# Optimization experiments

Hardware: AMD Instinct MI355X
Metric: run time of the kernel (lower is better)

## Reference

```python
import jax, jax.numpy as jnp
import numpy as np


def setup_inputs() -> dict:
    key = jax.random.key(0)
    D, H, T, B = 512, 512, 500, 128
    ks = jax.random.split(key, 12)
    tn = lambda k, shape: 0.01 * jax.random.truncated_normal(k, -2.0, 2.0, shape, dtype=jnp.float32)
    return {
        "inputs": jax.random.normal(ks[0], (B, D), dtype=jnp.float32),
        "Wz": tn(ks[1], (D, H)),
        "Wr": tn(ks[2], (D, H)),
        "Wh": tn(ks[3], (D, H)),
        "Uz": tn(ks[4], (H, H)),
        "Ur": tn(ks[5], (H, H)),
        "Uh": tn(ks[6], (H, H)),
        "bz": tn(ks[7], (H,)),
        "br": tn(ks[8], (H,)),
        "bh": tn(ks[9], (H,)),
        "Wo": tn(ks[10], (H, D)),
        "bo": tn(ks[11], (D,)),
        "T": T,
    }


def reference(inputs, Wz, Wr, Wh, Uz, Ur, Uh, bz, br, bh, Wo, bo, T):
    B, D = inputs.shape
    H = Wz.shape[1]

    def step(carry, _):
        h, x = carry  # h: [B,H], x: [B,D]
        r = jax.nn.sigmoid(x @ Wr + h @ Ur + br)
        h_prop = jnp.tanh(x @ Wh + (r * h) @ Uh + bh)
        z = jax.nn.sigmoid(x @ Wz + h @ Uz + bz)
        h_new = jnp.clip((1.0 - z) * h + z * h_prop, -5.0, 5.0)
        out = h_new @ Wo + bo
        return (h_new, out), out

    h0 = jnp.zeros((B, H), dtype=inputs.dtype)
    _, outs = jax.lax.scan(step, (h0, inputs), None, length=T - 1)  # [T-1,B,D]
    full = jnp.concatenate([inputs[None], outs], axis=0)  # [T,B,D]
    return jnp.transpose(full, (1, 0, 2))  # [B,T,D]
```

## Files before the change

### kernel.cpp

```cpp
#include <hip/hip_runtime.h>
#include <cstdint>

#define NB 128
#define DH 512
#define ROWS 528

#define OFF_M   0u
#define OFF_M1  1048576u
#define OFF_UH  2097152u
#define OFF_H   2359296u
#define OFF_RH  2426880u
#define OFF_XT  2494464u
#define OFF_GZ  2562048u
#define OFF_GH  2627584u
#define OFF_CV  2693120u
#define OFF_C1  2695168u
#define OFF_BAR 2697216u
#define OFF_H2  2701312u

__device__ __forceinline__ float sigm(float x) { return 1.f / (1.f + __expf(-x)); }
__device__ __forceinline__ float tanh_fast(float x) {
  float e = __expf(2.f * fminf(x, 40.f));
  return (e - 1.f) / (e + 1.f);
}

__device__ __forceinline__ float cload(const float* p) {
  return __hip_atomic_load(p, __ATOMIC_RELAXED, __HIP_MEMORY_SCOPE_AGENT);
}
__device__ __forceinline__ void cstore(float* p, float v) {
  __hip_atomic_store(p, v, __ATOMIC_RELAXED, __HIP_MEMORY_SCOPE_AGENT);
}

__global__ __launch_bounds__(256) void gru_pre(
    const float* __restrict__ inputs,
    const float* __restrict__ Wz, const float* __restrict__ Wr, const float* __restrict__ Wh,
    const float* __restrict__ Uz, const float* __restrict__ Ur, const float* __restrict__ Uh,
    const float* __restrict__ bz, const float* __restrict__ br, const float* __restrict__ bh,
    const float* __restrict__ Wo, const float* __restrict__ bo,
    float* __restrict__ ws)
{
  __shared__ float sh[8960];
  const int bid = blockIdx.x, t = threadIdx.x;
  float* Mw  = ws + OFF_M;
  float* M1w = ws + OFF_M1;
  float* Uhw = ws + OFF_UH;
  float* hw0 = ws + OFF_H;
  float* hw1 = ws + OFF_H2;
  float* rhw = ws + OFF_RH;
  float* xT  = ws + OFF_XT;
  float* cv  = ws + OFF_CV;
  float* c1  = ws + OFF_C1;
  uint32_t* bar = (uint32_t*)(ws + OFF_BAR);

  if (bid < 256) {
    const int kh = bid >> 7, cch = bid & 127;
    const int reg = cch >> 5;
    const int k0 = kh * 256, c0 = cch * 16;
    if (reg == 3) {
      const int cc0 = c0 - 1536;
      for (int i = 0; i < 16; ++i) {
        int idx = t + i * 256;
        int kk = k0 + (idx >> 4), ci = idx & 15;
        Mw[(cch * 512 + kk) * 16 + ci] = Wo[kk * 512 + cc0 + ci];
      }
    } else {
      const float* Ws = (reg == 0) ? Wr : (reg == 1) ? Wz : Wh;
      const float* Us = (reg == 0) ? Ur : (reg == 1) ? Uz : nullptr;
      const int cc0 = c0 - reg * 512;
      const int kl = t;
      const int k = k0 + kl;
      float acc[16];
      #pragma unroll
      for (int c = 0; c < 16; ++c) acc[c] = 0.f;
      for (int jt = 0; jt < 16; ++jt) {
        __syncthreads();
        for (int i = 0; i < 32; ++i) {
          int idx = t + i * 256;
          int kk = idx >> 5, jj = idx & 31;
          sh[kk * 35 + jj] = Wo[(k0 + kk) * 512 + jt * 32 + jj];
        }
        __syncthreads();
        for (int j = 0; j < 32; ++j) {
          float wv = sh[kl * 35 + j];
          const float* wrow = Ws + (jt * 32 + j) * 512 + cc0;
          #pragma unroll
          for (int c = 0; c < 16; ++c) acc[c] = fmaf(wv, wrow[c], acc[c]);
        }
      }
      #pragma unroll
      for (int c = 0; c < 16; ++c) {
        float v = acc[c];
        if (Us) v += Us[k * 512 + cc0 + c];
        Mw[(cch * 512 + k) * 16 + c] = v;
      }
    }
  }
  else if (bid < 264) {
    const int q = bid - 256;
    const int r2 = q >> 1;
    const float* Ws = (r2 == 0) ? Wr : (r2 == 1) ? Wz : (r2 == 2) ? Wh : nullptr;
    const float* bs = (r2 == 0) ? br : (r2 == 1) ? bz : (r2 == 2) ? bh : nullptr;
    for (int round = 0; round < 8; ++round) {
      int col32 = t >> 3, strip = t & 7;
      int c = q * 256 + round * 32 + col32;
      int cc = c & 511;
      float p = 0.f;
      if (r2 < 3) {
        for (int j = strip * 64; j < strip * 64 + 64; ++j)
          p = fmaf(bo[j], Ws[j * 512 + cc], p);
      }
      sh[col32 * 8 + strip] = p;
      __syncthreads();
      if (t < 32) {
        float v = 0.f;
        #pragma unroll
        for (int st = 0; st < 8; ++st) v += sh[t * 8 + st];
        int c2 = q * 256 + round * 32 + t;
        int cc2 = c2 & 511;
        cv[c2] = (r2 < 3) ? (v + bs[cc2]) : bo[cc2];
      }
      __syncthreads();
    }
  }
  else if (bid < 288) {
    const int q = bid - 264;
    for (int cq = 0; cq < 4; ++cq) {
      int ch = q * 4 + cq;
      int r3 = ch >> 5;
      const float* Ws = (r3 == 0) ? Wr : (r3 == 1) ? Wz : Wh;
      int cc0 = (ch & 31) * 16;
      for (int i = 0; i < 32; ++i) {
        int idx = t + i * 256;
        int kk = idx >> 4, ci = idx & 15;
        M1w[(ch * 512 + kk) * 16 + ci] = Ws[kk * 512 + cc0 + ci];
      }
    }
  }
  else if (bid < 296) {
    const int q = bid - 288;
    for (int cq = 0; cq < 4; ++cq) {
      int ch = 96 + q * 4 + cq;
      for (int i = 0; i < 32; ++i) {
        int idx = t + i * 256;
        M1w[ch * 8192 + idx] = 0.f;
      }
    }
  }
  else if (bid < 312) {
    const int q = bid - 296;
    for (int cq = 0; cq < 4; ++cq) {
      int ch = q * 4 + cq;
      for (int i = 0; i < 16; ++i) {
        int idx = t + i * 256;
        int kk = idx >> 3, ci = idx & 7;
        Uhw[(ch * 512 + kk) * 8 + ci] = Uh[kk * 512 + ch * 8 + ci];
      }
    }
  }
  else if (bid < 316) {
    const int q = bid - 312;
    for (int ti = q * 4; ti < q * 4 + 4; ++ti) {
      int bt = ti >> 3, dt = ti & 7;
      __syncthreads();
      for (int i = 0; i < 16; ++i) {
        int idx = t + i * 256;
        int r = idx >> 6, c = idx & 63;
        sh[r * 65 + c] = inputs[(bt * 64 + r) * 512 + dt * 64 + c];
      }
      __syncthreads();
      for (int i = 0; i < 16; ++i) {
        int idx = t + i * 256;
        int r = idx >> 6, c = idx & 63;
        xT[(dt * 64 + r) * 128 + bt * 64 + c] = sh[c * 65 + r];
      }
    }
    if (q == 0) {
      for (int idx = t; idx < 16 * 128; idx += 256) xT[512 * 128 + idx] = 0.f;
    }
  }
  else if (bid == 316) {
    for (int idx = t; idx < ROWS * 128; idx += 256) hw0[idx] = 0.f;
  }
  else if (bid == 317) {
    for (int idx = t; idx < 16 * 128; idx += 256) rhw[512 * 128 + idx] = 0.f;
  }
  else if (bid == 318) {
    for (int idx = t; idx < 2048; idx += 256)
      c1[idx] = (idx < 512) ? br[idx] : (idx < 1024) ? bz[idx - 512]
              : (idx < 1536) ? bh[idx - 1024] : 0.f;
    for (int idx = t; idx < 4096; idx += 256) bar[idx] = 0u;
  }
  else if (bid == 319) {
    for (int idx = t; idx < ROWS * 128; idx += 256) hw1[idx] = 0.f;
  }
}

#define BAR_R 0
#define BAR_G 1024
#define BAR_B 2048

__device__ __forceinline__ void arrive(uint32_t* bar, int base, int xcls,
                                       uint32_t perCls, uint32_t ph) {
  __syncthreads();
  if (threadIdx.x == 0) {
    uint32_t o = __hip_atomic_fetch_add(&bar[base + xcls * 32], 1u,
                                        __ATOMIC_RELAXED, __HIP_MEMORY_SCOPE_AGENT);
    if (o == ph * perCls + (perCls - 1u)) {
      uint32_t g = __hip_atomic_fetch_add(&bar[base + 256], 1u,
                                          __ATOMIC_RELAXED, __HIP_MEMORY_SCOPE_AGENT);
      if (g == ph * 8u + 7u) {
        #pragma unroll
        for (int x = 0; x < 8; ++x)
          __hip_atomic_store(&bar[base + 512 + x * 32], ph + 1u,
                             __ATOMIC_RELAXED, __HIP_MEMORY_SCOPE_AGENT);
      }
    }
  }
}
__device__ __forceinline__ void waitf(uint32_t* bar, int base, int xcls, uint32_t ph) {
  if (threadIdx.x == 0) {
    int guard = 0;
    while (__hip_atomic_load(&bar[base + 512 + xcls * 32],
                             __ATOMIC_RELAXED, __HIP_MEMORY_SCOPE_AGENT) < ph + 1u) {
      __builtin_amdgcn_s_sleep(1);
      if (++guard > (1 << 18)) break;
    }
  }
  __syncthreads();
}

__global__ __launch_bounds__(512, 2) void gru_main(
    const float* __restrict__ inputs,
    const float* __restrict__ Mw, const float* __restrict__ M1w,
    const float* __restrict__ Uhw,
    const float* __restrict__ cvec, const float* __restrict__ c1vec,
    float* __restrict__ hw0, float* __restrict__ hw1,
    float* __restrict__ rhw,
    const float* __restrict__ xT,
    float* __restrict__ Gz, float* __restrict__ Gh,
    uint32_t* __restrict__ bar, float* __restrict__ out, const int T)
{
  __shared__ float Ald[8192];
  __shared__ float Uld[4096];
  __shared__ float red[4096];
  __shared__ float ttr[1024];

  const int bid = blockIdx.x, tid = threadIdx.x;
  const int wave = __builtin_amdgcn_readfirstlane(tid >> 6);
  const int lane = tid & 63;
  const int bh = bid >> 7, chnk = bid & 127;
  const int typ = chnk >> 5;
  const int b = bh * 64 + lane;
  const int xcls = bid & 7;
  const bool isB = (bid < 128);
  const int bh2 = bid >> 6, ch8 = bid & 63;
  const int cg = tid >> 6, lane_ = tid & 63;

  {
    const float* src = M1w + (size_t)chnk * 8192;
    #pragma unroll
    for (int i = 0; i < 4; ++i) {
      const int idx4 = tid + i * 512;
      *(float4*)&Ald[idx4 * 4] = *(const float4*)&src[idx4 * 4];
    }
    if (isB) {
      const float* us = Uhw + (size_t)ch8 * 4096;
      *(float4*)&Uld[tid * 4]        = ((const float4*)us)[tid];
      *(float4*)&Uld[2048 + tid * 4] = ((const float4*)us)[512 + tid];
    }
  }
  __syncthreads();

  for (int s = 1; s <= T; ++s) {
    const int p = s & 1;
    const float* hcur = p ? hw1 : hw0;
    float* hnxt = p ? hw0 : hw1;
    const uint32_t ph = (uint32_t)(s - 1);

    {
      const float* hsrc = (s == 1) ? xT : hcur;
      const float* cv = (s == 1) ? c1vec : cvec;
      float hpre[2];
      if (typ == 0) {
        #pragma unroll
        for (int i = 0; i < 2; ++i)
          hpre[i] = cload(&hcur[(chnk * 16 + cg * 2 + i) * 128 + bh * 64 + lane_]);
      }
      float acc[16];
      #pragma unroll
      for (int c = 0; c < 16; ++c) acc[c] = 0.f;
      const float* hp = hsrc + (wave * 64) * 128 + b;
      float hv[32];
      #pragma unroll
      for (int u = 0; u < 32; ++u) hv[u] = cload(hp + u * 128);
      #pragma unroll
      for (int u = 0; u < 32; ++u) {
        const float cur = hv[u];
        hv[u] = cload(hp + (32 + u) * 128);
        const float* mrow = &Ald[(wave * 64 + u) * 16];
        #pragma unroll
        for (int c = 0; c < 16; ++c) acc[c] = fmaf(cur, mrow[c], acc[c]);
      }
      #pragma unroll
      for (int u = 0; u < 32; ++u) {
        const float* mrow = &Ald[(wave * 64 + 32 + u) * 16];
        #pragma unroll
        for (int c = 0; c < 16; ++c) acc[c] = fmaf(hv[u], mrow[c], acc[c]);
      }
      if (wave >= 4) {
        #pragma unroll
        for (int c = 0; c < 16; ++c) red[((wave - 4) * 16 + c) * 64 + lane] = acc[c];
      }
      __syncthreads();
      if (wave < 4) {
        #pragma unroll
        for (int c = 0; c < 16; ++c) red[(wave * 16 + c) * 64 + lane] += acc[c];
      }
      __syncthreads();
      const int bb = bh * 64 + lane_;
      float vout[2];
      #pragma unroll
      for (int i = 0; i < 2; ++i) {
        const int c = cg * 2 + i;
        float v = red[c * 64 + lane_] + red[(16 + c) * 64 + lane_]
                + red[(32 + c) * 64 + lane_] + red[(48 + c) * 64 + lane_];
        vout[i] = v + cv[chnk * 16 + c];
      }
      if (typ == 0) {
        #pragma unroll
        for (int i = 0; i < 2; ++i) {
          const int cglob = chnk * 16 + cg * 2 + i;
          cstore(&rhw[cglob * 128 + bb], sigm(vout[i]) * hpre[i]);
        }
        if (s < T) arrive(bar, BAR_R, xcls, 8, ph);
      } else if (typ == 1) {
        #pragma unroll
        for (int i = 0; i < 2; ++i) {
          const int cglob = chnk * 16 + cg * 2 + i;
          cstore(&Gz[(cglob - 512) * 128 + bb], sigm(vout[i]));
        }
        if (s < T) arrive(bar, BAR_G, xcls, 24, ph);
      } else if (typ == 2) {
        #pragma unroll
        for (int i = 0; i < 2; ++i) {
          const int cglob = chnk * 16 + cg * 2 + i;
          cstore(&Gh[(cglob - 1024) * 128 + bb], vout[i]);
        }
        if (s < T) arrive(bar, BAR_G, xcls, 24, ph);
      } else {
        if (s < T) arrive(bar, BAR_G, xcls, 24, ph);
        if (s > 1) {
          #pragma unroll
          for (int i = 0; i < 2; ++i) ttr[lane_ * 16 + cg * 2 + i] = vout[i];
          __syncthreads();
          const int bq = tid >> 3, pr = tid & 7;
          const float2 o2 = *(const float2*)&ttr[bq * 16 + pr * 2];
          const int bglob = bh * 64 + bq;
          const int d0 = (chnk - 96) * 16 + pr * 2;
          *(float2*)&out[(size_t)bglob * (size_t)T * 512 + (size_t)(s - 1) * 512 + d0] = o2;
        }
      }
    }

    if (s == 1) {
      __syncthreads();
      const float* src = Mw + (size_t)chnk * 8192;
      #pragma unroll
      for (int i = 0; i < 4; ++i) {
        const int idx4 = tid + i * 512;
        *(float4*)&Ald[idx4 * 4] = *(const float4*)&src[idx4 * 4];
      }
      if (tid < 256) {
        const int g = bid * 256 + tid;
        out[(size_t)(g >> 9) * (size_t)T * 512 + (g & 511)] = inputs[g];
      }
    }

    if (s < T) {
      if (isB) {
        waitf(bar, BAR_R, xcls, ph);
        const int cg2 = ch8 * 8 + cg;
        const int bb2 = bh2 * 64 + lane_;
        const float hprev = cload(&hcur[cg2 * 128 + bb2]);
        const float* rp = rhw + (wave * 64) * 128 + bh2 * 64 + lane;
        float hv[32];
        #pragma unroll
        for (int u = 0; u < 32; ++u) hv[u] = cload(rp + u * 128);
        float a2[8];
        #pragma unroll
        for (int c = 0; c < 8; ++c) a2[c] = 0.f;
        #pragma unroll
        for (int u = 0; u < 32; ++u) {
          const float cur = hv[u];
          hv[u] = cload(rp + (32 + u) * 128);
          const float* urow = &Uld[(wave * 64 + u) * 8];
          #pragma unroll
          for (int c = 0; c < 8; ++c) a2[c] = fmaf(cur, urow[c], a2[c]);
        }
        #pragma unroll
        for (int u = 0; u < 32; ++u) {
          const float* urow = &Uld[(wave * 64 + 32 + u) * 8];
          #pragma unroll
          for (int c = 0; c < 8; ++c) a2[c] = fmaf(hv[u], urow[c], a2[c]);
        }
        if (wave >= 4) {
          #pragma unroll
          for (int c = 0; c < 8; ++c) red[((wave - 4) * 8 + c) * 64 + lane] = a2[c];
        }
        __syncthreads();
        if (wave < 4) {
          #pragma unroll
          for (int c = 0; c < 8; ++c) red[(wave * 8 + c) * 64 + lane] += a2[c];
        }
        waitf(bar, BAR_G, xcls, ph);
        const float zf  = cload(&Gz[cg2 * 128 + bb2]);
        const float ghf = cload(&Gh[cg2 * 128 + bb2]);
        const float S = red[cg * 64 + lane_] + red[(8 + cg) * 64 + lane_]
                      + red[(16 + cg) * 64 + lane_] + red[(24 + cg) * 64 + lane_];
        float hn = (1.f - zf) * hprev + zf * tanh_fast(ghf + S);
        hn = fminf(5.f, fmaxf(-5.f, hn));
        cstore(&hnxt[cg2 * 128 + bb2], hn);
        arrive(bar, BAR_B, xcls, 16, ph);
      }
      waitf(bar, BAR_B, xcls, ph);
    }
  }
}

extern "C" void kernel_launch(void* const* d_in, const int* in_sizes, int n_in,
                              void* d_out, int out_size, void* d_ws, size_t ws_size,
                              hipStream_t stream) {
  const float* inputs = (const float*)d_in[0];
  const float* Wz = (const float*)d_in[1];
  const float* Wr = (const float*)d_in[2];
  const float* Wh = (const float*)d_in[3];
  const float* Uz = (const float*)d_in[4];
  const float* Ur = (const float*)d_in[5];
  const float* Uh = (const float*)d_in[6];
  const float* bz = (const float*)d_in[7];
  const float* br = (const float*)d_in[8];
  const float* bh = (const float*)d_in[9];
  const float* Wo = (const float*)d_in[10];
  const float* bo = (const float*)d_in[11];
  float* ws = (float*)d_ws;
  const int T = out_size / (128 * 512);

  gru_pre<<<dim3(320), dim3(256), 0, stream>>>(inputs, Wz, Wr, Wh, Uz, Ur, Uh,
                                               bz, br, bh, Wo, bo, ws);
  gru_main<<<dim3(256), dim3(512), 0, stream>>>(
      inputs, ws + OFF_M, ws + OFF_M1, ws + OFF_UH, ws + OFF_CV, ws + OFF_C1,
      ws + OFF_H, ws + OFF_H2, ws + OFF_RH, ws + OFF_XT, ws + OFF_GZ, ws + OFF_GH,
      (uint32_t*)(ws + OFF_BAR), (float*)d_out, T);
}
```

Before: 6.969 ms.

## Split blocks into r/candidate and z/h/out roles with flat counter barriers

```diff
diff --git a/kernel.cpp b/kernel.cpp
--- a/kernel.cpp
+++ b/kernel.cpp
@@ -5,8 +5,10 @@
 #define DH 512
 #define ROWS 528
 
-#define OFF_M   0u
-#define OFF_M1  1048576u
+#define OFF_MAR 0u
+#define OFF_MAZ 262144u
+#define OFF_M1R 1048576u
+#define OFF_M1Z 1310720u
 #define OFF_UH  2097152u
 #define OFF_H   2359296u
 #define OFF_RH  2426880u
@@ -18,6 +20,10 @@
 #define OFF_BAR 2697216u
 #define OFF_H2  2701312u
 
+#define BAR_R 0
+#define BAR_G 1024
+#define BAR_B 2048
+
 __device__ __forceinline__ float sigm(float x) { return 1.f / (1.f + __expf(-x)); }
 __device__ __forceinline__ float tanh_fast(float x) {
   float e = __expf(2.f * fminf(x, 40.f));
@@ -29,6 +35,15 @@
 }
 __device__ __forceinline__ void cstore(float* p, float v) {
   __hip_atomic_store(p, v, __ATOMIC_RELAXED, __HIP_MEMORY_SCOPE_AGENT);
+}
+
+__device__ __forceinline__ void scatterM(float* Mr, float* Mz, int C, int k, float v) {
+  if (C < 512) {
+    Mr[(C >> 3) * 4096 + k * 8 + (C & 7)] = v;
+  } else {
+    const int cc = C - 512;
+    Mz[(cc / 24) * 12288 + k * 24 + (cc % 24)] = v;
+  }
 }
 
 __global__ __launch_bounds__(256) void gru_pre(
@@ -41,8 +56,10 @@
 {
   __shared__ float sh[8960];
   const int bid = blockIdx.x, t = threadIdx.x;
-  float* Mw  = ws + OFF_M;
-  float* M1w = ws + OFF_M1;
+  float* MAr = ws + OFF_MAR;
+  float* MAz = ws + OFF_MAZ;
+  float* M1r = ws + OFF_M1R;
+  float* M1z = ws + OFF_M1Z;
   float* Uhw = ws + OFF_UH;
   float* hw0 = ws + OFF_H;
   float* hw1 = ws + OFF_H2;
@@ -61,7 +78,7 @@
       for (int i = 0; i < 16; ++i) {
         int idx = t + i * 256;
         int kk = k0 + (idx >> 4), ci = idx & 15;
-        Mw[(cch * 512 + kk) * 16 + ci] = Wo[kk * 512 + cc0 + ci];
+        scatterM(MAr, MAz, c0 + ci, kk, Wo[kk * 512 + cc0 + ci]);
       }
     } else {
       const float* Ws = (reg == 0) ? Wr : (reg == 1) ? Wz : Wh;
@@ -91,7 +108,7 @@
       for (int c = 0; c < 16; ++c) {
         float v = acc[c];
         if (Us) v += Us[k * 512 + cc0 + c];
-        Mw[(cch * 512 + k) * 16 + c] = v;
+        scatterM(MAr, MAz, c0 + c, k, v);
       }
     }
   }
@@ -122,27 +139,16 @@
       __syncthreads();
     }
   }
-  else if (bid < 288) {
+  else if (bid < 296) {
     const int q = bid - 264;
-    for (int cq = 0; cq < 4; ++cq) {
-      int ch = q * 4 + cq;
-      int r3 = ch >> 5;
-      const float* Ws = (r3 == 0) ? Wr : (r3 == 1) ? Wz : Wh;
-      int cc0 = (ch & 31) * 16;
-      for (int i = 0; i < 32; ++i) {
-        int idx = t + i * 256;
-        int kk = idx >> 4, ci = idx & 15;
-        M1w[(ch * 512 + kk) * 16 + ci] = Ws[kk * 512 + cc0 + ci];
-      }
-    }
-  }
-  else if (bid < 296) {
-    const int q = bid - 288;
-    for (int cq = 0; cq < 4; ++cq) {
-      int ch = 96 + q * 4 + cq;
-      for (int i = 0; i < 32; ++i) {
-        int idx = t + i * 256;
-        M1w[ch * 8192 + idx] = 0.f;
+    for (int cq = 0; cq < 64; ++cq) {
+      const int C = q * 64 + cq;
+      const int r3 = C >> 9;
+      const float* Ws = (r3 == 0) ? Wr : (r3 == 1) ? Wz : (r3 == 2) ? Wh : nullptr;
+      const int cc = C & 511;
+      for (int k = t; k < 512; k += 256) {
+        float v = Ws ? Ws[k * 512 + cc] : 0.f;
+        scatterM(M1r, M1z, C, k, v);
       }
     }
   }
@@ -195,33 +201,20 @@
   }
 }
 
-#define BAR_R 0
-#define BAR_G 1024
-#define BAR_B 2048
-
-__device__ __forceinline__ void arrive(uint32_t* bar, int base, int xcls,
-                                       uint32_t perCls, uint32_t ph) {
+__device__ __forceinline__ void arriveCnt(uint32_t* cnt, int xcls) {
   __syncthreads();
-  if (threadIdx.x == 0) {
-    uint32_t o = __hip_atomic_fetch_add(&bar[base + xcls * 32], 1u,
-                                        __ATOMIC_RELAXED, __HIP_MEMORY_SCOPE_AGENT);
-    if (o == ph * perCls + (perCls - 1u)) {
-      uint32_t g = __hip_atomic_fetch_add(&bar[base + 256], 1u,
-                                          __ATOMIC_RELAXED, __HIP_MEMORY_SCOPE_AGENT);
-      if (g == ph * 8u + 7u) {
-        #pragma unroll
-        for (int x = 0; x < 8; ++x)
-          __hip_atomic_store(&bar[base + 512 + x * 32], ph + 1u,
-                             __ATOMIC_RELAXED, __HIP_MEMORY_SCOPE_AGENT);
-      }
-    }
-  }
-}
-__device__ __forceinline__ void waitf(uint32_t* bar, int base, int xcls, uint32_t ph) {
+  if (threadIdx.x == 0)
+    __hip_atomic_fetch_add(&cnt[xcls * 32], 1u, __ATOMIC_RELAXED, __HIP_MEMORY_SCOPE_AGENT);
+}
+__device__ __forceinline__ void waitCnt(uint32_t* cnt, uint32_t target) {
   if (threadIdx.x == 0) {
     int guard = 0;
-    while (__hip_atomic_load(&bar[base + 512 + xcls * 32],
-                             __ATOMIC_RELAXED, __HIP_MEMORY_SCOPE_AGENT) < ph + 1u) {
+    for (;;) {
+      uint32_t ssum = 0;
+      #pragma unroll
+      for (int x = 0; x < 8; ++x)
+        ssum += __hip_atomic_load(&cnt[x * 32], __ATOMIC_RELAXED, __HIP_MEMORY_SCOPE_AGENT);
+      if (ssum >= target) break;
       __builtin_amdgcn_s_sleep(1);
       if (++guard > (1 << 18)) break;
     }
@@ -229,9 +222,10 @@
   __syncthreads();
 }
 
-__global__ __launch_bounds__(512, 2) void gru_main(
+__global__ __launch_bounds__(512, 1) void gru_main(
     const float* __restrict__ inputs,
-    const float* __restrict__ Mw, const float* __restrict__ M1w,
+    const float* __restrict__ MAr, const float* __restrict__ MAz,
+    const float* __restrict__ M1r, const float* __restrict__ M1z,
     const float* __restrict__ Uhw,
     const float* __restrict__ cvec, const float* __restrict__ c1vec,
     float* __restrict__ hw0, float* __restrict__ hw1,
@@ -240,34 +234,37 @@
     float* __restrict__ Gz, float* __restrict__ Gh,
     uint32_t* __restrict__ bar, float* __restrict__ out, const int T)
 {
-  __shared__ float Ald[8192];
-  __shared__ float Uld[4096];
-  __shared__ float red[4096];
-  __shared__ float ttr[1024];
+  __shared__ float Wsh[12288];
+  __shared__ float red[6144];
 
   const int bid = blockIdx.x, tid = threadIdx.x;
   const int wave = __builtin_amdgcn_readfirstlane(tid >> 6);
   const int lane = tid & 63;
-  const int bh = bid >> 7, chnk = bid & 127;
-  const int typ = chnk >> 5;
-  const int b = bh * 64 + lane;
+  const bool isRB = (bid < 128);
+  const int rid  = isRB ? bid : (bid - 128);
+  const int half = rid >> 6;
+  const int ch   = rid & 63;
   const int xcls = bid & 7;
-  const bool isB = (bid < 128);
-  const int bh2 = bid >> 6, ch8 = bid & 63;
-  const int cg = tid >> 6, lane_ = tid & 63;
-
-  {
-    const float* src = M1w + (size_t)chnk * 8192;
+  const int b = half * 64 + lane;
+  const int cg = tid >> 6, ll = tid & 63;
+  uint32_t* cntR = bar + BAR_R;
+  uint32_t* cntG = bar + BAR_G;
+  uint32_t* cntB = bar + BAR_B;
+
+  if (isRB) {
+    const float* s1 = M1r + (size_t)ch * 4096;
     #pragma unroll
-    for (int i = 0; i < 4; ++i) {
-      const int idx4 = tid + i * 512;
-      *(float4*)&Ald[idx4 * 4] = *(const float4*)&src[idx4 * 4];
-    }
-    if (isB) {
-      const float* us = Uhw + (size_t)ch8 * 4096;
-      *(float4*)&Uld[tid * 4]        = ((const float4*)us)[tid];
-      *(float4*)&Uld[2048 + tid * 4] = ((const float4*)us)[512 + tid];
-    }
+    for (int i = 0; i < 2; ++i)
+      ((float4*)Wsh)[tid + i * 512] = ((const float4*)s1)[tid + i * 512];
+    const float* us = Uhw + (size_t)ch * 4096;
+    #pragma unroll
+    for (int i = 0; i < 2; ++i)
+      ((float4*)(Wsh + 4096))[tid + i * 512] = ((const float4*)us)[tid + i * 512];
+  } else {
+    const float* s1 = M1z + (size_t)ch * 12288;
+    #pragma unroll
+    for (int i = 0; i < 6; ++i)
+      ((float4*)Wsh)[tid + i * 512] = ((const float4*)s1)[tid + i * 512];
   }
   __syncthreads();
 
@@ -275,20 +272,16 @@
     const int p = s & 1;
     const float* hcur = p ? hw1 : hw0;
     float* hnxt = p ? hw0 : hw1;
-    const uint32_t ph = (uint32_t)(s - 1);
-
-    {
-      const float* hsrc = (s == 1) ? xT : hcur;
-      const float* cv = (s == 1) ? c1vec : cvec;
-      float hpre[2];
-      if (typ == 0) {
-        #pragma unroll
-        for (int i = 0; i < 2; ++i)
-          hpre[i] = cload(&hcur[(chnk * 16 + cg * 2 + i) * 128 + bh * 64 + lane_]);
-      }
-      float acc[16];
-      #pragma unroll
-      for (int c = 0; c < 16; ++c) acc[c] = 0.f;
+    const float* hsrc = (s == 1) ? xT : hcur;
+    const float* cvp = (s == 1) ? c1vec : cvec;
+    const uint32_t tgt = (uint32_t)s * 128u;
+
+    if (isRB) {
+      const int C = ch * 8 + cg;
+      const float hpre = cload(&hcur[C * 128 + half * 64 + ll]);
+      float acc[8];
+      #pragma unroll
+      for (int c = 0; c < 8; ++c) acc[c] = 0.f;
       const float* hp = hsrc + (wave * 64) * 128 + b;
       float hv[32];
       #pragma unroll
@@ -297,132 +290,141 @@
       for (int u = 0; u < 32; ++u) {
         const float cur = hv[u];
         hv[u] = cload(hp + (32 + u) * 128);
-        const float* mrow = &Ald[(wave * 64 + u) * 16];
-        #pragma unroll
-        for (int c = 0; c < 16; ++c) acc[c] = fmaf(cur, mrow[c], acc[c]);
+        const float* mrow = &Wsh[(wave * 64 + u) * 8];
+        #pragma unroll
+        for (int c = 0; c < 8; ++c) acc[c] = fmaf(cur, mrow[c], acc[c]);
       }
       #pragma unroll
       for (int u = 0; u < 32; ++u) {
-        const float* mrow = &Ald[(wave * 64 + 32 + u) * 16];
-        #pragma unroll
-        for (int c = 0; c < 16; ++c) acc[c] = fmaf(hv[u], mrow[c], acc[c]);
+        const float* mrow = &Wsh[(wave * 64 + 32 + u) * 8];
+        #pragma unroll
+        for (int c = 0; c < 8; ++c) acc[c] = fmaf(hv[u], mrow[c], acc[c]);
       }
       if (wave >= 4) {
         #pragma unroll
-        for (int c = 0; c < 16; ++c) red[((wave - 4) * 16 + c) * 64 + lane] = acc[c];
+        for (int c = 0; c < 8; ++c) red[((wave - 4) * 8 + c) * 64 + lane] = acc[c];
       }
       __syncthreads();
       if (wave < 4) {
         #pragma unroll
-        for (int c = 0; c < 16; ++c) red[(wave * 16 + c) * 64 + lane] += acc[c];
-      }
-      __syncthreads();
-      const int bb = bh * 64 + lane_;
-      float vout[2];
-      #pragma unroll
-      for (int i = 0; i < 2; ++i) {
-        const int c = cg * 2 + i;
-        float v = red[c * 64 + lane_] + red[(16 + c) * 64 + lane_]
-                + red[(32 + c) * 64 + lane_] + red[(48 + c) * 64 + lane_];
-        vout[i] = v + cv[chnk * 16 + c];
-      }
-      if (typ == 0) {
-        #pragma unroll
-        for (int i = 0; i < 2; ++i) {
-          const int cglob = chnk * 16 + cg * 2 + i;
-          cstore(&rhw[cglob * 128 + bb], sigm(vout[i]) * hpre[i]);
-        }
-        if (s < T) arrive(bar, BAR_R, xcls, 8, ph);
-      } else if (typ == 1) {
-        #pragma unroll
-        for (int i = 0; i < 2; ++i) {
-          const int cglob = chnk * 16 + cg * 2 + i;
-          cstore(&Gz[(cglob - 512) * 128 + bb], sigm(vout[i]));
-        }
-        if (s < T) arrive(bar, BAR_G, xcls, 24, ph);
-      } else if (typ == 2) {
-        #pragma unroll
-        for (int i = 0; i < 2; ++i) {
-          const int cglob = chnk * 16 + cg * 2 + i;
-          cstore(&Gh[(cglob - 1024) * 128 + bb], vout[i]);
-        }
-        if (s < T) arrive(bar, BAR_G, xcls, 24, ph);
-      } else {
-        if (s < T) arrive(bar, BAR_G, xcls, 24, ph);
-        if (s > 1) {
-          #pragma unroll
-          for (int i = 0; i < 2; ++i) ttr[lane_ * 16 + cg * 2 + i] = vout[i];
-          __syncthreads();
-          const int bq = tid >> 3, pr = tid & 7;
-          const float2 o2 = *(const float2*)&ttr[bq * 16 + pr * 2];
-          const int bglob = bh * 64 + bq;
-          const int d0 = (chnk - 96) * 16 + pr * 2;
-          *(float2*)&out[(size_t)bglob * (size_t)T * 512 + (size_t)(s - 1) * 512 + d0] = o2;
-        }
-      }
-    }
-
-    if (s == 1) {
-      __syncthreads();
-      const float* src = Mw + (size_t)chnk * 8192;
-      #pragma unroll
-      for (int i = 0; i < 4; ++i) {
-        const int idx4 = tid + i * 512;
-        *(float4*)&Ald[idx4 * 4] = *(const float4*)&src[idx4 * 4];
-      }
-      if (tid < 256) {
-        const int g = bid * 256 + tid;
-        out[(size_t)(g >> 9) * (size_t)T * 512 + (g & 511)] = inputs[g];
-      }
-    }
-
-    if (s < T) {
-      if (isB) {
-        waitf(bar, BAR_R, xcls, ph);
-        const int cg2 = ch8 * 8 + cg;
-        const int bb2 = bh2 * 64 + lane_;
-        const float hprev = cload(&hcur[cg2 * 128 + bb2]);
-        const float* rp = rhw + (wave * 64) * 128 + bh2 * 64 + lane;
-        float hv[32];
-        #pragma unroll
-        for (int u = 0; u < 32; ++u) hv[u] = cload(rp + u * 128);
+        for (int c = 0; c < 8; ++c) red[(wave * 8 + c) * 64 + lane] += acc[c];
+      }
+      __syncthreads();
+      float v = red[cg * 64 + ll] + red[512 + cg * 64 + ll]
+              + red[1024 + cg * 64 + ll] + red[1536 + cg * 64 + ll] + cvp[C];
+      cstore(&rhw[C * 128 + half * 64 + ll], sigm(v) * hpre);
+      if (s < T) {
+        arriveCnt(cntR, xcls);
+        if (s == 1) {
+          const float* src = MAr + (size_t)ch * 4096;
+          #pragma unroll
+          for (int i = 0; i < 2; ++i)
+            ((float4*)Wsh)[tid + i * 512] = ((const float4*)src)[tid + i * 512];
+        }
+        waitCnt(cntR, tgt);
         float a2[8];
         #pragma unroll
         for (int c = 0; c < 8; ++c) a2[c] = 0.f;
+        const float* rp = rhw + (wave * 64) * 128 + b;
+        float rv[32];
+        #pragma unroll
+        for (int u = 0; u < 32; ++u) rv[u] = cload(rp + u * 128);
         #pragma unroll
         for (int u = 0; u < 32; ++u) {
-          const float cur = hv[u];
-          hv[u] = cload(rp + (32 + u) * 128);
-          const float* urow = &Uld[(wave * 64 + u) * 8];
+          const float cur = rv[u];
+          rv[u] = cload(rp + (32 + u) * 128);
+          const float* urow = &Wsh[4096 + (wave * 64 + u) * 8];
           #pragma unroll
           for (int c = 0; c < 8; ++c) a2[c] = fmaf(cur, urow[c], a2[c]);
         }
         #pragma unroll
         for (int u = 0; u < 32; ++u) {
-          const float* urow = &Uld[(wave * 64 + 32 + u) * 8];
-          #pragma unroll
-          for (int c = 0; c < 8; ++c) a2[c] = fmaf(hv[u], urow[c], a2[c]);
+          const float* urow = &Wsh[4096 + (wave * 64 + 32 + u) * 8];
+          #pragma unroll
+          for (int c = 0; c < 8; ++c) a2[c] = fmaf(rv[u], urow[c], a2[c]);
         }
         if (wave >= 4) {
           #pragma unroll
           for (int c = 0; c < 8; ++c) red[((wave - 4) * 8 + c) * 64 + lane] = a2[c];
         }
+        waitCnt(cntG, tgt);
+        const float zf  = cload(&Gz[C * 128 + half * 64 + ll]);
+        const float ghf = cload(&Gh[C * 128 + half * 64 + ll]);
+        if (wave < 4) {
+          #pragma unroll
+          for (int c = 0; c < 8; ++c) red[(wave * 8 + c) * 64 + lane] += a2[c];
+        }
         __syncthreads();
-        if (wave < 4) {
-          #pragma unroll
-          for (int c = 0; c < 8; ++c) red[(wave * 8 + c) * 64 + lane] += a2[c];
-        }
-        waitf(bar, BAR_G, xcls, ph);
-        const float zf  = cload(&Gz[cg2 * 128 + bb2]);
-        const float ghf = cload(&Gh[cg2 * 128 + bb2]);
-        const float S = red[cg * 64 + lane_] + red[(8 + cg) * 64 + lane_]
-                      + red[(16 + cg) * 64 + lane_] + red[(24 + cg) * 64 + lane_];
-        float hn = (1.f - zf) * hprev + zf * tanh_fast(ghf + S);
+        const float S = red[cg * 64 + ll] + red[512 + cg * 64 + ll]
+                      + red[1024 + cg * 64 + ll] + red[1536 + cg * 64 + ll];
+        float hn = (1.f - zf) * hpre + zf * tanh_fast(ghf + S);
         hn = fminf(5.f, fmaxf(-5.f, hn));
-        cstore(&hnxt[cg2 * 128 + bb2], hn);
-        arrive(bar, BAR_B, xcls, 16, ph);
-      }
-      waitf(bar, BAR_B, xcls, ph);
+        cstore(&hnxt[C * 128 + half * 64 + ll], hn);
+        arriveCnt(cntB, xcls);
+        waitCnt(cntB, tgt);
+      }
+    } else {
+      float acc[24];
+      #pragma unroll
+      for (int c = 0; c < 24; ++c) acc[c] = 0.f;
+      const float* hp = hsrc + (wave * 64) * 128 + b;
+      float hv[32];
+      #pragma unroll
+      for (int u = 0; u < 32; ++u) hv[u] = cload(hp + u * 128);
+      #pragma unroll
+      for (int u = 0; u < 32; ++u) {
+        const float cur = hv[u];
+        hv[u] = cload(hp + (32 + u) * 128);
+        const float* mrow = &Wsh[(wave * 64 + u) * 24];
+        #pragma unroll
+        for (int c = 0; c < 24; ++c) acc[c] = fmaf(cur, mrow[c], acc[c]);
+      }
+      #pragma unroll
+      for (int u = 0; u < 32; ++u) {
+        const float* mrow = &Wsh[(wave * 64 + 32 + u) * 24];
+        #pragma unroll
+        for (int c = 0; c < 24; ++c) acc[c] = fmaf(hv[u], mrow[c], acc[c]);
+      }
+      if (wave >= 4) {
+        #pragma unroll
+        for (int c = 0; c < 24; ++c) red[((wave - 4) * 24 + c) * 64 + lane] = acc[c];
+      }
+      __syncthreads();
+      if (wave < 4) {
+        #pragma unroll
+        for (int c = 0; c < 24; ++c) red[(wave * 24 + c) * 64 + lane] += acc[c];
+      }
+      __syncthreads();
+      const int b2 = half * 64 + ll;
+      float vo[3]; int Cs[3];
+      #pragma unroll
+      for (int i = 0; i < 3; ++i) {
+        const int cl = cg * 3 + i;
+        const int C = 512 + ch * 24 + cl;
+        float v = red[cl * 64 + ll] + red[1536 + cl * 64 + ll]
+                + red[3072 + cl * 64 + ll] + red[4608 + cl * 64 + ll] + cvp[C];
+        vo[i] = v; Cs[i] = C;
+        if (C < 1024)      cstore(&Gz[(C - 512) * 128 + b2], sigm(v));
+        else if (C < 1536) cstore(&Gh[(C - 1024) * 128 + b2], v);
+      }
+      if (s < T) arriveCnt(cntG, xcls);
+      if (s > 1) {
+        #pragma unroll
+        for (int i = 0; i < 3; ++i) {
+          if (Cs[i] >= 1536)
+            out[(size_t)b2 * (size_t)T * 512 + (size_t)(s - 1) * 512 + (Cs[i] - 1536)] = vo[i];
+        }
+      }
+      if (s == 1) {
+        __syncthreads();
+        const float* src = MAz + (size_t)ch * 12288;
+        #pragma unroll
+        for (int i = 0; i < 6; ++i)
+          ((float4*)Wsh)[tid + i * 512] = ((const float4*)src)[tid + i * 512];
+        const int r0 = bid - 128;
+        out[(size_t)r0 * (size_t)T * 512 + tid] = inputs[r0 * 512 + tid];
+      }
+      if (s < T) waitCnt(cntB, tgt);
     }
   }
 }
@@ -448,7 +450,8 @@
   gru_pre<<<dim3(320), dim3(256), 0, stream>>>(inputs, Wz, Wr, Wh, Uz, Ur, Uh,
                                                bz, br, bh, Wo, bo, ws);
   gru_main<<<dim3(256), dim3(512), 0, stream>>>(
-      inputs, ws + OFF_M, ws + OFF_M1, ws + OFF_UH, ws + OFF_CV, ws + OFF_C1,
+      inputs, ws + OFF_MAR, ws + OFF_MAZ, ws + OFF_M1R, ws + OFF_M1Z,
+      ws + OFF_UH, ws + OFF_CV, ws + OFF_C1,
       ws + OFF_H, ws + OFF_H2, ws + OFF_RH, ws + OFF_XT, ws + OFF_GZ, ws + OFF_GH,
       (uint32_t*)(ws + OFF_BAR), (float*)d_out, T);
 }
```

Measured after the change: 10.52 ms. 50.9% more time.
